# Optimization experiments

Hardware: AMD Instinct MI355X
Metric: run time of the kernel (lower is better)

The kernel has to match this reference:

```python
import jax, jax.numpy as jnp
import numpy as np

B, T, D_MODEL, HEAD = 8, 2048, 1024, 64
NEG = -1e9  # finite mask fill; exp underflows to 0 in softmax, avoids inf/NaN


def setup_inputs() -> dict:
    key = jax.random.key(0)
    k1, k2, k3, k4, k5 = jax.random.split(key, 5)
    x = jax.random.normal(k1, (B, T, D_MODEL), dtype=jnp.float32)
    valid_lens = jax.random.randint(k2, (B,), 0, T)
    # nn.Linear(d_model, head_size, bias=False): y = x @ W, W: (d_model, head_size)
    s = 0.02
    Wq = jax.random.normal(k3, (D_MODEL, HEAD), dtype=jnp.float32) * s
    Wk = jax.random.normal(k4, (D_MODEL, HEAD), dtype=jnp.float32) * s
    Wv = jax.random.normal(k5, (D_MODEL, HEAD), dtype=jnp.float32) * s
    return {"x": x, "Wq": Wq, "Wk": Wk, "Wv": Wv, "valid_lens": valid_lens}


def reference(x, Wq, Wk, Wv, valid_lens):
    # x: (B, T, D), projections -> (B, T, H)
    q = jnp.einsum("btd,dh->bth", x, Wq)
    k = jnp.einsum("btd,dh->bth", x, Wk)
    v = jnp.einsum("btd,dh->bth", x, Wv)
    scale = k.shape[-1] ** -0.5
    wei = jnp.einsum("bqh,bkh->bqk", q, k) * scale  # (B, T, T)

    t = jnp.arange(T)
    causal = t[None, :] <= t[:, None]                     # (T, T) lower-tri
    valid = t[None, :] < valid_lens[:, None]              # (B, T)
    mask = causal[None, :, :] & valid[:, :, None] & valid[:, None, :]  # (B, T, T)

    wei = jnp.where(mask, wei, NEG)
    attn = jax.nn.softmax(wei, axis=2)
    # rows with no valid key get all-masked scores -> original code zeros them out
    row_all_masked = ~jnp.any(mask, axis=2)               # (B, T)
    attn = jnp.where(row_all_masked[:, :, None], 0.0, attn)
    # dropout(p=0.0) == identity
    out = jnp.einsum("bqk,bkh->bqh", attn, v)             # (B, T, H)
    return out
```

## Files before the change

### kernel.cpp

```cpp
#include <hip/hip_runtime.h>
#include <hip/hip_bf16.h>
#include <stdint.h>

#define T_   2048
#define DM_  1024
#define HD_  64
#define NROW 16384
#define SPLIT 4
#define BM   32
#define BK   64

typedef __attribute__((ext_vector_type(8))) __bf16 bf16x8;
typedef __attribute__((ext_vector_type(4))) __bf16 bf16x4;
typedef __attribute__((ext_vector_type(4))) float  f32x4;

__global__ void wconv_k(const float* __restrict__ Wq, const float* __restrict__ Wk,
                        const float* __restrict__ Wv, __bf16* __restrict__ wfrag) {
    int tid  = blockIdx.x * 256 + threadIdx.x;
    int lane = tid & 63;
    int t    = (tid >> 6) % 12;
    int kc   = tid / (12 * 64);
    int c = lane & 15, g = lane >> 4;
    int n = t * 16 + c;
    const float* W = (n < 64) ? Wq : (n < 128) ? Wk : Wv;
    int col = n & 63;
    int k0  = kc * 32 + g * 8;
    __bf16* dst = wfrag + (size_t)tid * 8;
#pragma unroll
    for (int j = 0; j < 8; ++j) dst[j] = (__bf16)W[(k0 + j) * HD_ + col];
}

__global__ __launch_bounds__(256, 2) void proj_k(const float* __restrict__ x,
        const __bf16* __restrict__ wfrag, __bf16* __restrict__ Qb,
        __bf16* __restrict__ Kb, __bf16* __restrict__ Vt) {
    __shared__ __bf16 abuf[2][BM][72];
    __shared__ __bf16 bbuf[2][2][12][512];
    int tid  = threadIdx.x;
    int lane = tid & 63, wave = tid >> 6;
    int mh = wave >> 1, th = wave & 1;
    int c = lane & 15, g = lane >> 4;
    int row0 = blockIdx.x * BM;
    int ar = tid >> 3, a0 = (tid & 7) * 8;
    const float* xrow = x + (size_t)(row0 + ar) * DM_ + a0;

    f32x4 acc[6];
#pragma unroll
    for (int t = 0; t < 6; ++t) acc[t] = (f32x4)0.f;

    {
#pragma unroll
        for (int i = 0; i < 6; ++i) {
            int p = wave * 6 + i;
            int kh = p / 12, tt = p % 12;
            const __bf16* src = wfrag + ((size_t)kh * 12 + tt) * 512 + lane * 8;
            __builtin_amdgcn_global_load_lds(
                (const __attribute__((address_space(1))) void*)src,
                (__attribute__((address_space(3))) void*)&bbuf[0][kh][tt][0], 16, 0, 0);
        }
        f32x4 x0 = *(const f32x4*)(xrow);
        f32x4 x1 = *(const f32x4*)(xrow + 4);
        bf16x8 a;
#pragma unroll
        for (int j = 0; j < 4; ++j) { a[j] = (__bf16)x0[j]; a[4 + j] = (__bf16)x1[j]; }
        *(bf16x8*)&abuf[0][ar][a0] = a;
    }

    for (int kk = 0; kk < 16; ++kk) {
        int buf = kk & 1, nb = buf ^ 1;
        __syncthreads();
        f32x4 x0, x1;
        bool hn = (kk + 1) < 16;
        if (hn) {
            const float* xp = xrow + (kk + 1) * BK;
            x0 = *(const f32x4*)(xp);
            x1 = *(const f32x4*)(xp + 4);
#pragma unroll
            for (int i = 0; i < 6; ++i) {
                int p = wave * 6 + i;
                int kh = p / 12, tt = p % 12;
                const __bf16* src = wfrag + (((size_t)(kk + 1) * 2 + kh) * 12 + tt) * 512 + lane * 8;
                __builtin_amdgcn_global_load_lds(
                    (const __attribute__((address_space(1))) void*)src,
                    (__attribute__((address_space(3))) void*)&bbuf[nb][kh][tt][0], 16, 0, 0);
            }
        }
#pragma unroll
        for (int kh = 0; kh < 2; ++kh) {
            bf16x8 af = *(const bf16x8*)&abuf[buf][mh * 16 + c][kh * 32 + g * 8];
#pragma unroll
            for (int t = 0; t < 6; ++t) {
                bf16x8 bfh = *(const bf16x8*)&bbuf[buf][kh][th * 6 + t][lane * 8];
                acc[t] = __builtin_amdgcn_mfma_f32_16x16x32_bf16(af, bfh, acc[t], 0, 0, 0);
            }
        }
        if (hn) {
            bf16x8 a;
#pragma unroll
            for (int j = 0; j < 4; ++j) { a[j] = (__bf16)x0[j]; a[4 + j] = (__bf16)x1[j]; }
            *(bf16x8*)&abuf[nb][ar][a0] = a;
        }
    }

#pragma unroll
    for (int t = 0; t < 6; ++t) {
        int tg = th * 6 + t;
        int n  = tg * 16 + c;
#pragma unroll
        for (int r = 0; r < 4; ++r) {
            int grow = row0 + mh * 16 + g * 4 + r;
            float v  = acc[t][r];
            if (n < 64)       Qb[(size_t)grow * HD_ + n] = (__bf16)(v * 0.18033688f);
            else if (n < 128) Kb[(size_t)grow * HD_ + (n - 64)] = (__bf16)v;
            else              Vt[(size_t)(grow >> 11) * (HD_ * T_) + (size_t)(n - 128) * T_ + (grow & 2047)] = (__bf16)v;
        }
    }
}

__global__ __launch_bounds__(128) void attn_k(const __bf16* __restrict__ Qb,
        const __bf16* __restrict__ Kb, const __bf16* __restrict__ Vt,
        float* __restrict__ Opart, float* __restrict__ ml) {
    int split = blockIdx.x >> 9;
    int bid2  = blockIdx.x & 511;
    int half = bid2 >> 8, idx = bid2 & 255;
    int b = idx >> 5, p = idx & 31;
    int qb = half ? (63 - p) : p;
    int wave = threadIdx.x >> 6, lane = threadIdx.x & 63;
    int c = lane & 15, g = lane >> 4;
    int qg   = qb * 32 + wave * 16 + c;
    int tile = b * 128 + qb * 2 + wave;
    int nd2  = (qb + 2) >> 1;
    float m = -1e30f, lsum = 0.f;
    if (split < nd2) {
        const __bf16* qp = Qb + (size_t)(b * T_ + qg) * HD_ + g * 8;
        bf16x8 qf0 = *(const bf16x8*)qp;
        bf16x8 qf1 = *(const bf16x8*)(qp + 32);
        const __bf16* Kbase = Kb + (size_t)b * T_ * HD_;
        const __bf16* Vbase = Vt + (size_t)b * HD_ * T_;
        f32x4 o0 = (f32x4)0.f, o1 = (f32x4)0.f, o2 = (f32x4)0.f, o3 = (f32x4)0.f;
        __shared__ __bf16 plds[2][16][72];
        __bf16 (*pl)[72] = plds[wave];
        for (int kt = split; kt < nd2; kt += SPLIT) {
            int kv0 = kt * 64;
            const __bf16* kp = Kbase + (size_t)(kv0 + c) * HD_ + g * 8;
            bf16x8 ka00 = *(const bf16x8*)(kp);
            bf16x8 ka01 = *(const bf16x8*)(kp + 32);
            bf16x8 ka10 = *(const bf16x8*)(kp + 16 * HD_);
            bf16x8 ka11 = *(const bf16x8*)(kp + 16 * HD_ + 32);
            bf16x8 kb00 = *(const bf16x8*)(kp + 32 * HD_);
            bf16x8 kb01 = *(const bf16x8*)(kp + 32 * HD_ + 32);
            bf16x8 kb10 = *(const bf16x8*)(kp + 48 * HD_);
            bf16x8 kb11 = *(const bf16x8*)(kp + 48 * HD_ + 32);
            f32x4 sa0 = (f32x4)0.f, sa1 = (f32x4)0.f, sb0 = (f32x4)0.f, sb1 = (f32x4)0.f;
            sa0 = __builtin_amdgcn_mfma_f32_16x16x32_bf16(ka00, qf0, sa0, 0, 0, 0);
            sa0 = __builtin_amdgcn_mfma_f32_16x16x32_bf16(ka01, qf1, sa0, 0, 0, 0);
            sa1 = __builtin_amdgcn_mfma_f32_16x16x32_bf16(ka10, qf0, sa1, 0, 0, 0);
            sa1 = __builtin_amdgcn_mfma_f32_16x16x32_bf16(ka11, qf1, sa1, 0, 0, 0);
            sb0 = __builtin_amdgcn_mfma_f32_16x16x32_bf16(kb00, qf0, sb0, 0, 0, 0);
            sb0 = __builtin_amdgcn_mfma_f32_16x16x32_bf16(kb01, qf1, sb0, 0, 0, 0);
            sb1 = __builtin_amdgcn_mfma_f32_16x16x32_bf16(kb10, qf0, sb1, 0, 0, 0);
            sb1 = __builtin_amdgcn_mfma_f32_16x16x32_bf16(kb11, qf1, sb1, 0, 0, 0);
            float s[16];
#pragma unroll
            for (int r = 0; r < 4; ++r) {
                s[r] = sa0[r]; s[4 + r] = sa1[r]; s[8 + r] = sb0[r]; s[12 + r] = sb1[r];
            }
            if (kt == nd2 - 1) {
#pragma unroll
                for (int i = 0; i < 16; ++i) {
                    int kv = kv0 + (i >> 2) * 16 + g * 4 + (i & 3);
                    if (kv > qg) s[i] = -1e30f;
                }
            }
            float tm = s[0];
#pragma unroll
            for (int i = 1; i < 16; ++i) tm = fmaxf(tm, s[i]);
            tm = fmaxf(tm, __shfl_xor(tm, 16));
            tm = fmaxf(tm, __shfl_xor(tm, 32));
            float mn = fmaxf(m, tm);
            float al = __builtin_amdgcn_exp2f(m - mn);
            float ps = 0.f;
#pragma unroll
            for (int i = 0; i < 16; ++i) { s[i] = __builtin_amdgcn_exp2f(s[i] - mn); ps += s[i]; }
            ps += __shfl_xor(ps, 16);
            ps += __shfl_xor(ps, 32);
            lsum = lsum * al + ps;
            m = mn;
            o0 *= al; o1 *= al; o2 *= al; o3 *= al;
#pragma unroll
            for (int mt = 0; mt < 4; ++mt) {
                bf16x4 pv;
#pragma unroll
                for (int r = 0; r < 4; ++r) pv[r] = (__bf16)s[mt * 4 + r];
                *(bf16x4*)&pl[c][mt * 16 + g * 4] = pv;
            }
            bf16x8 pf0 = *(const bf16x8*)&pl[c][g * 8];
            bf16x8 pf1 = *(const bf16x8*)&pl[c][32 + g * 8];
            const __bf16* vp = Vbase + (size_t)c * T_ + kv0 + g * 8;
            bf16x8 v0a = *(const bf16x8*)(vp);
            bf16x8 v1a = *(const bf16x8*)(vp + 16 * T_);
            bf16x8 v2a = *(const bf16x8*)(vp + 32 * T_);
            bf16x8 v3a = *(const bf16x8*)(vp + 48 * T_);
            bf16x8 v0b = *(const bf16x8*)(vp + 32);
            bf16x8 v1b = *(const bf16x8*)(vp + 16 * T_ + 32);
            bf16x8 v2b = *(const bf16x8*)(vp + 32 * T_ + 32);
            bf16x8 v3b = *(const bf16x8*)(vp + 48 * T_ + 32);
            o0 = __builtin_amdgcn_mfma_f32_16x16x32_bf16(v0a, pf0, o0, 0, 0, 0);
            o1 = __builtin_amdgcn_mfma_f32_16x16x32_bf16(v1a, pf0, o1, 0, 0, 0);
            o2 = __builtin_amdgcn_mfma_f32_16x16x32_bf16(v2a, pf0, o2, 0, 0, 0);
            o3 = __builtin_amdgcn_mfma_f32_16x16x32_bf16(v3a, pf0, o3, 0, 0, 0);
            o0 = __builtin_amdgcn_mfma_f32_16x16x32_bf16(v0b, pf1, o0, 0, 0, 0);
            o1 = __builtin_amdgcn_mfma_f32_16x16x32_bf16(v1b, pf1, o1, 0, 0, 0);
            o2 = __builtin_amdgcn_mfma_f32_16x16x32_bf16(v2b, pf1, o2, 0, 0, 0);
            o3 = __builtin_amdgcn_mfma_f32_16x16x32_bf16(v3b, pf1, o3, 0, 0, 0);
        }
        float* op = Opart + ((size_t)tile * SPLIT + split) * 1024 + c * 64 + g * 4;
        *(f32x4*)(op)      = o0;
        *(f32x4*)(op + 16) = o1;
        *(f32x4*)(op + 32) = o2;
        *(f32x4*)(op + 48) = o3;
    }
    if (g == 0) {
        float* mlp = ml + ((size_t)tile * SPLIT + split) * 32 + c * 2;
        mlp[0] = m; mlp[1] = lsum;
    }
}

__global__ __launch_bounds__(256) void comb_k(const float* __restrict__ Opart,
        const float* __restrict__ ml, const int* __restrict__ vlen,
        float* __restrict__ out) {
    int tile = blockIdx.x;
    int b  = tile >> 7;
    int q0 = (tile & 127) * 16;
    int q  = threadIdx.x >> 4;
    int d0 = (threadIdx.x & 15) * 4;
    int qg = q0 + q;
    const float* mlp = ml + (size_t)tile * SPLIT * 32 + q * 2;
    float mj[SPLIT], lj[SPLIT];
#pragma unroll
    for (int j = 0; j < SPLIT; ++j) { mj[j] = mlp[j * 32]; lj[j] = mlp[j * 32 + 1]; }
    float M = fmaxf(fmaxf(mj[0], mj[1]), fmaxf(mj[2], mj[3]));
    f32x4 acc = (f32x4)0.f;
    float L = 0.f;
#pragma unroll
    for (int j = 0; j < SPLIT; ++j) {
        if (lj[j] > 0.f) {
            float sc = __builtin_amdgcn_exp2f(mj[j] - M);
            L += lj[j] * sc;
            f32x4 ov = *(const f32x4*)(Opart + ((size_t)tile * SPLIT + j) * 1024 + q * 64 + d0);
            acc += ov * sc;
        }
    }
    float inv = (qg < vlen[b]) ? 1.f / L : 0.f;
    f32x4 r = acc * inv;
    *(f32x4*)(out + ((size_t)(b * T_) + qg) * HD_ + d0) = r;
}

extern "C" void kernel_launch(void* const* d_in, const int* in_sizes, int n_in,
                              void* d_out, int out_size, void* d_ws, size_t ws_size,
                              hipStream_t stream) {
    const float* x   = (const float*)d_in[0];
    const float* Wq  = (const float*)d_in[1];
    const float* Wk  = (const float*)d_in[2];
    const float* Wv  = (const float*)d_in[3];
    const int*   vln = (const int*)d_in[4];
    float* out = (float*)d_out;

    __bf16* Qb    = (__bf16*)d_ws;
    __bf16* Kb    = Qb + (size_t)NROW * HD_;
    __bf16* Vt    = Kb + (size_t)NROW * HD_;
    __bf16* wfrag = Vt + (size_t)NROW * HD_;
    float*  Opart = (float*)(wfrag + 24576 * 8);
    float*  mlbuf = Opart + (size_t)1024 * SPLIT * 1024;

    wconv_k<<<96, 256, 0, stream>>>(Wq, Wk, Wv, wfrag);
    proj_k <<<512, 256, 0, stream>>>(x, wfrag, Qb, Kb, Vt);
    attn_k <<<512 * SPLIT, 128, 0, stream>>>(Qb, Kb, Vt, Opart, mlbuf);
    comb_k <<<1024, 256, 0, stream>>>(Opart, mlbuf, vln, out);
}
```

Measured before the change: 155.5 us.

## Switch attention to 32x32 MFMA tiles with register shuffle instead of LDS

Rewrites the attention kernel so each single-wave block processes a 32-query tile using 32x32x16 bf16 MFMAs, with 32-key steps. The P matrix is repacked for the PV product through cross-half lane shuffles instead of an LDS round trip. The KV split factor doubles to 8, and the combine kernel is reworked to match a new transposed partial-output layout. This removes shared-memory traffic and raises parallelism, but it adds more partial outputs to merge and uses smaller per-iteration key tiles.

```diff
diff --git a/kernel.cpp b/kernel.cpp
--- a/kernel.cpp
+++ b/kernel.cpp
@@ -6,13 +6,21 @@
 #define DM_  1024
 #define HD_  64
 #define NROW 16384
-#define SPLIT 4
+#define SPLIT 8
 #define BM   32
 #define BK   64
 
-typedef __attribute__((ext_vector_type(8))) __bf16 bf16x8;
-typedef __attribute__((ext_vector_type(4))) __bf16 bf16x4;
-typedef __attribute__((ext_vector_type(4))) float  f32x4;
+typedef __attribute__((ext_vector_type(8)))  __bf16 bf16x8;
+typedef __attribute__((ext_vector_type(4)))  __bf16 bf16x4;
+typedef __attribute__((ext_vector_type(4)))  float  f32x4;
+typedef __attribute__((ext_vector_type(16))) float  f32x16;
+typedef __attribute__((ext_vector_type(4)))  unsigned int u32x4;
+
+static __device__ __forceinline__ unsigned pk2(float a, float b) {
+    unsigned short ua = __builtin_bit_cast(unsigned short, (__bf16)a);
+    unsigned short ub = __builtin_bit_cast(unsigned short, (__bf16)b);
+    return (unsigned)ua | ((unsigned)ub << 16);
+}
 
 __global__ void wconv_k(const float* __restrict__ Wq, const float* __restrict__ Wk,
                         const float* __restrict__ Wv, __bf16* __restrict__ wfrag) {
@@ -116,111 +124,103 @@
     }
 }
 
-__global__ __launch_bounds__(128) void attn_k(const __bf16* __restrict__ Qb,
+__global__ __launch_bounds__(64, 3) void attn_k(const __bf16* __restrict__ Qb,
         const __bf16* __restrict__ Kb, const __bf16* __restrict__ Vt,
         float* __restrict__ Opart, float* __restrict__ ml) {
     int split = blockIdx.x >> 9;
-    int bid2  = blockIdx.x & 511;
-    int half = bid2 >> 8, idx = bid2 & 255;
-    int b = idx >> 5, p = idx & 31;
-    int qb = half ? (63 - p) : p;
-    int wave = threadIdx.x >> 6, lane = threadIdx.x & 63;
-    int c = lane & 15, g = lane >> 4;
-    int qg   = qb * 32 + wave * 16 + c;
-    int tile = b * 128 + qb * 2 + wave;
-    int nd2  = (qb + 2) >> 1;
+    int rest  = blockIdx.x & 511;
+    int b = rest >> 6, p = rest & 63;
+    int qt = (p & 1) ? (63 - (p >> 1)) : (p >> 1);
+    int lane = threadIdx.x & 63;
+    int low = lane & 31, h = lane >> 5;
+    int q0 = qt * 32, qg = q0 + low;
+    int t32 = b * 64 + qt;
+    int nd = qt + 1;
     float m = -1e30f, lsum = 0.f;
-    if (split < nd2) {
-        const __bf16* qp = Qb + (size_t)(b * T_ + qg) * HD_ + g * 8;
-        bf16x8 qf0 = *(const bf16x8*)qp;
-        bf16x8 qf1 = *(const bf16x8*)(qp + 32);
+    f32x16 oa = (f32x16)0.f, ob = (f32x16)0.f;
+    if (split < nd) {
+        const __bf16* qp = Qb + (size_t)(b * T_ + qg) * HD_ + h * 8;
+        bf16x8 qf0 = *(const bf16x8*)(qp);
+        bf16x8 qf1 = *(const bf16x8*)(qp + 16);
+        bf16x8 qf2 = *(const bf16x8*)(qp + 32);
+        bf16x8 qf3 = *(const bf16x8*)(qp + 48);
         const __bf16* Kbase = Kb + (size_t)b * T_ * HD_;
         const __bf16* Vbase = Vt + (size_t)b * HD_ * T_;
-        f32x4 o0 = (f32x4)0.f, o1 = (f32x4)0.f, o2 = (f32x4)0.f, o3 = (f32x4)0.f;
-        __shared__ __bf16 plds[2][16][72];
-        __bf16 (*pl)[72] = plds[wave];
-        for (int kt = split; kt < nd2; kt += SPLIT) {
-            int kv0 = kt * 64;
-            const __bf16* kp = Kbase + (size_t)(kv0 + c) * HD_ + g * 8;
-            bf16x8 ka00 = *(const bf16x8*)(kp);
-            bf16x8 ka01 = *(const bf16x8*)(kp + 32);
-            bf16x8 ka10 = *(const bf16x8*)(kp + 16 * HD_);
-            bf16x8 ka11 = *(const bf16x8*)(kp + 16 * HD_ + 32);
-            bf16x8 kb00 = *(const bf16x8*)(kp + 32 * HD_);
-            bf16x8 kb01 = *(const bf16x8*)(kp + 32 * HD_ + 32);
-            bf16x8 kb10 = *(const bf16x8*)(kp + 48 * HD_);
-            bf16x8 kb11 = *(const bf16x8*)(kp + 48 * HD_ + 32);
-            f32x4 sa0 = (f32x4)0.f, sa1 = (f32x4)0.f, sb0 = (f32x4)0.f, sb1 = (f32x4)0.f;
-            sa0 = __builtin_amdgcn_mfma_f32_16x16x32_bf16(ka00, qf0, sa0, 0, 0, 0);
-            sa0 = __builtin_amdgcn_mfma_f32_16x16x32_bf16(ka01, qf1, sa0, 0, 0, 0);
-            sa1 = __builtin_amdgcn_mfma_f32_16x16x32_bf16(ka10, qf0, sa1, 0, 0, 0);
-            sa1 = __builtin_amdgcn_mfma_f32_16x16x32_bf16(ka11, qf1, sa1, 0, 0, 0);
-            sb0 = __builtin_amdgcn_mfma_f32_16x16x32_bf16(kb00, qf0, sb0, 0, 0, 0);
-            sb0 = __builtin_amdgcn_mfma_f32_16x16x32_bf16(kb01, qf1, sb0, 0, 0, 0);
-            sb1 = __builtin_amdgcn_mfma_f32_16x16x32_bf16(kb10, qf0, sb1, 0, 0, 0);
-            sb1 = __builtin_amdgcn_mfma_f32_16x16x32_bf16(kb11, qf1, sb1, 0, 0, 0);
-            float s[16];
-#pragma unroll
-            for (int r = 0; r < 4; ++r) {
-                s[r] = sa0[r]; s[4 + r] = sa1[r]; s[8 + r] = sb0[r]; s[12 + r] = sb1[r];
-            }
-            if (kt == nd2 - 1) {
-#pragma unroll
-                for (int i = 0; i < 16; ++i) {
-                    int kv = kv0 + (i >> 2) * 16 + g * 4 + (i & 3);
-                    if (kv > qg) s[i] = -1e30f;
+        for (int kt = split; kt < nd; kt += SPLIT) {
+            int kv0 = kt * 32;
+            const __bf16* kp = Kbase + (size_t)(kv0 + low) * HD_ + h * 8;
+            bf16x8 kf0 = *(const bf16x8*)(kp);
+            bf16x8 kf1 = *(const bf16x8*)(kp + 16);
+            bf16x8 kf2 = *(const bf16x8*)(kp + 32);
+            bf16x8 kf3 = *(const bf16x8*)(kp + 48);
+            const __bf16* vp = Vbase + (size_t)low * T_ + kv0 + h * 8;
+            bf16x8 va00 = *(const bf16x8*)(vp);
+            bf16x8 va01 = *(const bf16x8*)(vp + 16);
+            bf16x8 va10 = *(const bf16x8*)(vp + (size_t)32 * T_);
+            bf16x8 va11 = *(const bf16x8*)(vp + (size_t)32 * T_ + 16);
+            f32x16 st = (f32x16)0.f;
+            st = __builtin_amdgcn_mfma_f32_32x32x16_bf16(kf0, qf0, st, 0, 0, 0);
+            st = __builtin_amdgcn_mfma_f32_32x32x16_bf16(kf1, qf1, st, 0, 0, 0);
+            st = __builtin_amdgcn_mfma_f32_32x32x16_bf16(kf2, qf2, st, 0, 0, 0);
+            st = __builtin_amdgcn_mfma_f32_32x32x16_bf16(kf3, qf3, st, 0, 0, 0);
+            if (kt == nd - 1) {
+#pragma unroll
+                for (int r = 0; r < 16; ++r) {
+                    int kv = kv0 + (r & 3) + 8 * (r >> 2) + 4 * h;
+                    if (kv > qg) st[r] = -1e30f;
                 }
             }
-            float tm = s[0];
-#pragma unroll
-            for (int i = 1; i < 16; ++i) tm = fmaxf(tm, s[i]);
-            tm = fmaxf(tm, __shfl_xor(tm, 16));
+            float t0 = fmaxf(fmaxf(st[0], st[1]), fmaxf(st[2], st[3]));
+            float t1 = fmaxf(fmaxf(st[4], st[5]), fmaxf(st[6], st[7]));
+            float t2 = fmaxf(fmaxf(st[8], st[9]), fmaxf(st[10], st[11]));
+            float t3 = fmaxf(fmaxf(st[12], st[13]), fmaxf(st[14], st[15]));
+            float tm = fmaxf(fmaxf(t0, t1), fmaxf(t2, t3));
             tm = fmaxf(tm, __shfl_xor(tm, 32));
             float mn = fmaxf(m, tm);
             float al = __builtin_amdgcn_exp2f(m - mn);
-            float ps = 0.f;
-#pragma unroll
-            for (int i = 0; i < 16; ++i) { s[i] = __builtin_amdgcn_exp2f(s[i] - mn); ps += s[i]; }
-            ps += __shfl_xor(ps, 16);
-            ps += __shfl_xor(ps, 32);
-            lsum = lsum * al + ps;
             m = mn;
-            o0 *= al; o1 *= al; o2 *= al; o3 *= al;
-#pragma unroll
-            for (int mt = 0; mt < 4; ++mt) {
-                bf16x4 pv;
-#pragma unroll
-                for (int r = 0; r < 4; ++r) pv[r] = (__bf16)s[mt * 4 + r];
-                *(bf16x4*)&pl[c][mt * 16 + g * 4] = pv;
-            }
-            bf16x8 pf0 = *(const bf16x8*)&pl[c][g * 8];
-            bf16x8 pf1 = *(const bf16x8*)&pl[c][32 + g * 8];
-            const __bf16* vp = Vbase + (size_t)c * T_ + kv0 + g * 8;
-            bf16x8 v0a = *(const bf16x8*)(vp);
-            bf16x8 v1a = *(const bf16x8*)(vp + 16 * T_);
-            bf16x8 v2a = *(const bf16x8*)(vp + 32 * T_);
-            bf16x8 v3a = *(const bf16x8*)(vp + 48 * T_);
-            bf16x8 v0b = *(const bf16x8*)(vp + 32);
-            bf16x8 v1b = *(const bf16x8*)(vp + 16 * T_ + 32);
-            bf16x8 v2b = *(const bf16x8*)(vp + 32 * T_ + 32);
-            bf16x8 v3b = *(const bf16x8*)(vp + 48 * T_ + 32);
-            o0 = __builtin_amdgcn_mfma_f32_16x16x32_bf16(v0a, pf0, o0, 0, 0, 0);
-            o1 = __builtin_amdgcn_mfma_f32_16x16x32_bf16(v1a, pf0, o1, 0, 0, 0);
-            o2 = __builtin_amdgcn_mfma_f32_16x16x32_bf16(v2a, pf0, o2, 0, 0, 0);
-            o3 = __builtin_amdgcn_mfma_f32_16x16x32_bf16(v3a, pf0, o3, 0, 0, 0);
-            o0 = __builtin_amdgcn_mfma_f32_16x16x32_bf16(v0b, pf1, o0, 0, 0, 0);
-            o1 = __builtin_amdgcn_mfma_f32_16x16x32_bf16(v1b, pf1, o1, 0, 0, 0);
-            o2 = __builtin_amdgcn_mfma_f32_16x16x32_bf16(v2b, pf1, o2, 0, 0, 0);
-            o3 = __builtin_amdgcn_mfma_f32_16x16x32_bf16(v3b, pf1, o3, 0, 0, 0);
-        }
-        float* op = Opart + ((size_t)tile * SPLIT + split) * 1024 + c * 64 + g * 4;
-        *(f32x4*)(op)      = o0;
-        *(f32x4*)(op + 16) = o1;
-        *(f32x4*)(op + 32) = o2;
-        *(f32x4*)(op + 48) = o3;
-    }
-    if (g == 0) {
-        float* mlp = ml + ((size_t)tile * SPLIT + split) * 32 + c * 2;
+#pragma unroll
+            for (int r = 0; r < 16; ++r) st[r] = __builtin_amdgcn_exp2f(st[r] - mn);
+            float s0 = (st[0] + st[1]) + (st[2] + st[3]);
+            float s1 = (st[4] + st[5]) + (st[6] + st[7]);
+            float s2s = (st[8] + st[9]) + (st[10] + st[11]);
+            float s3 = (st[12] + st[13]) + (st[14] + st[15]);
+            lsum = lsum * al + ((s0 + s1) + (s2s + s3));
+            oa *= al; ob *= al;
+#pragma unroll
+            for (int s2 = 0; s2 < 2; ++s2) {
+                int base = 8 * s2;
+                unsigned w0 = pk2(st[base + 0], st[base + 1]);
+                unsigned w1 = pk2(st[base + 2], st[base + 3]);
+                unsigned w2 = pk2(st[base + 4], st[base + 5]);
+                unsigned w3 = pk2(st[base + 6], st[base + 7]);
+                unsigned x0 = h ? w0 : w2, x1 = h ? w1 : w3;
+                unsigned r0 = (unsigned)__shfl_xor((int)x0, 32);
+                unsigned r1 = (unsigned)__shfl_xor((int)x1, 32);
+                u32x4 wv;
+                wv.x = h ? r0 : w0; wv.y = h ? r1 : w1;
+                wv.z = h ? w2 : r0; wv.w = h ? w3 : r1;
+                bf16x8 pf = __builtin_bit_cast(bf16x8, wv);
+                if (s2 == 0) {
+                    oa = __builtin_amdgcn_mfma_f32_32x32x16_bf16(va00, pf, oa, 0, 0, 0);
+                    ob = __builtin_amdgcn_mfma_f32_32x32x16_bf16(va10, pf, ob, 0, 0, 0);
+                } else {
+                    oa = __builtin_amdgcn_mfma_f32_32x32x16_bf16(va01, pf, oa, 0, 0, 0);
+                    ob = __builtin_amdgcn_mfma_f32_32x32x16_bf16(va11, pf, ob, 0, 0, 0);
+                }
+            }
+        }
+        float* op = Opart + ((size_t)t32 * SPLIT + split) * 2048;
+#pragma unroll
+        for (int r = 0; r < 16; ++r) {
+            int d = (r & 3) + 8 * (r >> 2) + 4 * h;
+            op[d * 32 + low]        = oa[r];
+            op[(d + 32) * 32 + low] = ob[r];
+        }
+    }
+    lsum += __shfl_xor(lsum, 32);
+    if (h == 0) {
+        float* mlp = ml + ((size_t)t32 * SPLIT + split) * 64 + low * 2;
         mlp[0] = m; mlp[1] = lsum;
     }
 }
@@ -228,31 +228,34 @@
 __global__ __launch_bounds__(256) void comb_k(const float* __restrict__ Opart,
         const float* __restrict__ ml, const int* __restrict__ vlen,
         float* __restrict__ out) {
-    int tile = blockIdx.x;
-    int b  = tile >> 7;
-    int q0 = (tile & 127) * 16;
-    int q  = threadIdx.x >> 4;
-    int d0 = (threadIdx.x & 15) * 4;
-    int qg = q0 + q;
-    const float* mlp = ml + (size_t)tile * SPLIT * 32 + q * 2;
-    float mj[SPLIT], lj[SPLIT];
-#pragma unroll
-    for (int j = 0; j < SPLIT; ++j) { mj[j] = mlp[j * 32]; lj[j] = mlp[j * 32 + 1]; }
-    float M = fmaxf(fmaxf(mj[0], mj[1]), fmaxf(mj[2], mj[3]));
-    f32x4 acc = (f32x4)0.f;
-    float L = 0.f;
-#pragma unroll
-    for (int j = 0; j < SPLIT; ++j) {
-        if (lj[j] > 0.f) {
+    int t32 = blockIdx.x;
+    int b = t32 >> 6, q0 = (t32 & 63) * 32;
+    int vl = vlen[b];
+#pragma unroll
+    for (int u = threadIdx.x; u < 512; u += 256) {
+        int q = u & 31, dq = u >> 5;
+        const float* mlp = ml + (size_t)t32 * SPLIT * 64 + q * 2;
+        float mj[SPLIT], lj[SPLIT];
+#pragma unroll
+        for (int j = 0; j < SPLIT; ++j) { mj[j] = mlp[j * 64]; lj[j] = mlp[j * 64 + 1]; }
+        float M = mj[0];
+#pragma unroll
+        for (int j = 1; j < SPLIT; ++j) M = fmaxf(M, mj[j]);
+        f32x4 acc = (f32x4)0.f;
+        float L = 0.f;
+#pragma unroll
+        for (int j = 0; j < SPLIT; ++j) {
             float sc = __builtin_amdgcn_exp2f(mj[j] - M);
             L += lj[j] * sc;
-            f32x4 ov = *(const f32x4*)(Opart + ((size_t)tile * SPLIT + j) * 1024 + q * 64 + d0);
-            acc += ov * sc;
-        }
-    }
-    float inv = (qg < vlen[b]) ? 1.f / L : 0.f;
-    f32x4 r = acc * inv;
-    *(f32x4*)(out + ((size_t)(b * T_) + qg) * HD_ + d0) = r;
+            const float* op = Opart + ((size_t)t32 * SPLIT + j) * 2048 + dq * 128 + q;
+            acc[0] += op[0]  * sc;
+            acc[1] += op[32] * sc;
+            acc[2] += op[64] * sc;
+            acc[3] += op[96] * sc;
+        }
+        float inv = (q0 + q < vl) ? 1.f / L : 0.f;
+        *(f32x4*)(out + ((size_t)(b * T_) + q0 + q) * HD_ + dq * 4) = acc * inv;
+    }
 }
 
 extern "C" void kernel_launch(void* const* d_in, const int* in_sizes, int n_in,
@@ -270,10 +273,10 @@
     __bf16* Vt    = Kb + (size_t)NROW * HD_;
     __bf16* wfrag = Vt + (size_t)NROW * HD_;
     float*  Opart = (float*)(wfrag + 24576 * 8);
-    float*  mlbuf = Opart + (size_t)1024 * SPLIT * 1024;
+    float*  mlbuf = Opart + (size_t)512 * SPLIT * 2048;
 
     wconv_k<<<96, 256, 0, stream>>>(Wq, Wk, Wv, wfrag);
     proj_k <<<512, 256, 0, stream>>>(x, wfrag, Qb, Kb, Vt);
-    attn_k <<<512 * SPLIT, 128, 0, stream>>>(Qb, Kb, Vt, Opart, mlbuf);
-    comb_k <<<1024, 256, 0, stream>>>(Opart, mlbuf, vln, out);
-}
+    attn_k <<<512 * SPLIT, 64, 0, stream>>>(Qb, Kb, Vt, Opart, mlbuf);
+    comb_k <<<512, 256, 0, stream>>>(Opart, mlbuf, vln, out);
+}
```

New measurement: 156.1 us. About the same (+0.4%).
